# Performance work log

Measured on AMD Instinct MI355X. Metric: run time of the kernel, lower is better.

The kernel has to match this reference:

```python
import jax, jax.numpy as jnp
import numpy as np

B, M, FIN = 16, 49152, 16
F1, K = 32, 5
NNZ = 8 * M  # ~8 neighbors per vertex on a HEALPix sphere mesh


def setup_inputs() -> dict:
    key = jax.random.key(0)
    kx, kr, kc, kv, kw, kb = jax.random.split(key, 6)
    x = jax.random.normal(kx, (B, M, FIN), dtype=jnp.float32)
    rows = jax.random.randint(kr, (NNZ,), 0, M, dtype=jnp.int32)
    cols = jax.random.randint(kc, (NNZ,), 0, M, dtype=jnp.int32)
    # small values keep the order-K Chebyshev recurrence numerically tame
    vals = jax.random.normal(kv, (NNZ,), dtype=jnp.float32) * 0.1
    stddev = 1.0 / np.sqrt(FIN * (K + 0.5) / 2.0)
    kernel = jax.random.normal(kw, (FIN * K, F1), dtype=jnp.float32) * stddev
    bias = jax.random.uniform(kb, (1, 1, F1), dtype=jnp.float32) * 0.05
    return {"x": x, "rows": rows, "cols": cols, "vals": vals,
            "kernel": kernel, "bias": bias}


def reference(x, rows, cols, vals, kernel, bias):
    # x: [B, M, Fin]; sparse Laplacian L in COO (rows, cols, vals), shape [M, M]
    b, m, fin = x.shape
    k = kernel.shape[0] // fin

    def spmm(X):  # L @ X for X: [M, Fin*B]
        return jax.ops.segment_sum(vals[:, None] * X[cols], rows, num_segments=m)

    # x0: [M, Fin*B] exactly as the TF transpose/reshape does
    x0 = jnp.transpose(x, (1, 2, 0)).reshape(m, fin * b)
    xs = [x0]
    if k > 1:
        x1 = spmm(x0)
        xs.append(x1)
    for _ in range(2, k):
        x2 = 2.0 * spmm(x1) - x0
        xs.append(x2)
        x0, x1 = x1, x2
    # [K, M, Fin, B] -> [B, M, Fin, K] -> [B*M, Fin*K]
    xk = jnp.stack(xs, axis=0).reshape(k, m, fin, b)
    xk = jnp.transpose(xk, (3, 1, 2, 0)).reshape(b * m, fin * k)
    out = (xk @ kernel).reshape(b, m, -1)  # [B, M, F1]
    return out + bias
```

## Files before the change

kernel.cpp:

```cpp
#include <hip/hip_runtime.h>


constexpr int M   = 49152;
constexpr int B   = 16;
constexpr int FIN = 16;
constexpr int F1  = 32;
constexpr int K   = 5;
constexpr int XBS = M * FIN;
constexpr size_t SLICEB   = (size_t)M * 64;
constexpr size_t BUFBYTES = (size_t)M * 512;
constexpr int NBLK_M = M / 256;
constexpr int NHB = 64 * NBLK_M;

typedef short s16x8 __attribute__((ext_vector_type(8)));
typedef float f32x4 __attribute__((ext_vector_type(4)));
typedef unsigned int u32;
typedef unsigned long long u64;

#define DEVFN __device__ __forceinline__

DEVFN float lo2f(u32 d) {
  union { u32 u; float f; } v; v.u = d << 16; return v.f;
}
DEVFN float hi2f(u32 d) {
  union { u32 u; float f; } v; v.u = d & 0xffff0000u; return v.f;
}
DEVFN unsigned short f2bf(float f) {
  union { float f; u32 u; } v;
  v.f = f;
  u32 r = (v.u + 0x7FFFu + ((v.u >> 16) & 1u)) >> 16;
  return (unsigned short)r;
}


__global__ __launch_bounds__(256) void transform_x(const float* __restrict__ x,
                                                   char* __restrict__ x0b) {
  int lane = threadIdx.x & 63;
  int m = blockIdx.x * 4 + (threadIdx.x >> 6);
  int s = lane >> 3, i = lane & 7;
  int b = 2 * s + (i >> 2), f = (i & 3) * 4;
  float4 v = *(const float4*)(x + (size_t)b * XBS + (size_t)m * FIN + f);
  ushort4 r = make_ushort4(f2bf(v.x), f2bf(v.y), f2bf(v.z), f2bf(v.w));
  *(ushort4*)(x0b + (size_t)s * SLICEB + (size_t)m * 64 + i * 8) = r;
}


__global__ __launch_bounds__(256) void hist_kernel(const int* __restrict__ rows,
                                                   int* __restrict__ counts, int nnz) {
  int i = blockIdx.x * 256 + threadIdx.x;
  if (i < nnz) atomicAdd(&counts[rows[i]], 1);
}

DEVFN int wave_incl_scan(int v, int lane) {
#pragma unroll
  for (int off = 1; off < 64; off <<= 1) {
    int t = __shfl_up(v, off);
    if (lane >= off) v += t;
  }
  return v;
}

__global__ __launch_bounds__(1024) void scan_blocks(const int* __restrict__ src,
                                                    int* __restrict__ dst,
                                                    int* __restrict__ partials) {
  __shared__ int wsum[16];
  int tid = threadIdx.x, lane = tid & 63, w = tid >> 6;
  int i = blockIdx.x * 1024 + tid;
  int s = wave_incl_scan(src[i], lane);
  if (lane == 63) wsum[w] = s;
  __syncthreads();
  if (tid < 16) {
    int t = wsum[tid];
#pragma unroll
    for (int off = 1; off < 16; off <<= 1) {
      int u = __shfl_up(t, off);
      if (tid >= off) t += u;
    }
    wsum[tid] = t;
  }
  __syncthreads();
  int base = (w > 0) ? wsum[w - 1] : 0;
  s += base;
  dst[i + 1] = s;
  if (tid == 1023) partials[blockIdx.x] = s;
}

__global__ void scan_partials_kernel(int* __restrict__ partials,
                                     int* __restrict__ dst, int nblk) {
  int lane = threadIdx.x;
  int v = (lane < nblk) ? partials[lane] : 0;
  v = wave_incl_scan(v, lane);
  if (lane < nblk) partials[lane] = v;
  if (lane == 0) dst[0] = 0;
}

__global__ __launch_bounds__(1024) void scan_add_kernel(int* __restrict__ dst,
                                                        const int* __restrict__ partials) {
  if (blockIdx.x == 0) return;
  int i = blockIdx.x * 1024 + threadIdx.x;
  dst[i + 1] += partials[blockIdx.x - 1];
}

__global__ __launch_bounds__(256) void scatter_kernel(const int* __restrict__ rows,
                                                      const int* __restrict__ cols,
                                                      const float* __restrict__ vals,
                                                      const int* __restrict__ row_ptr,
                                                      int* __restrict__ fill,
                                                      u32* __restrict__ cvp, int nnz) {
  int i = blockIdx.x * 256 + threadIdx.x;
  if (i < nnz) {
    int r = rows[i];
    int pos = row_ptr[r] + atomicAdd(&fill[r], 1);
    cvp[pos] = ((u32)cols[i] << 16) | (u32)f2bf(vals[i]);
  }
}


__global__ __launch_bounds__(256) void deg_hist_blk(const int* __restrict__ counts,
                                                    int* __restrict__ blkhist) {
  __shared__ int lh[64];
  int tid = threadIdx.x;
  if (tid < 64) lh[tid] = 0;
  __syncthreads();
  int m = blockIdx.x * 256 + tid;
  atomicAdd(&lh[min(counts[m], 63)], 1);
  __syncthreads();
  if (tid < 64) blkhist[tid * NBLK_M + blockIdx.x] = lh[tid];
}

__global__ __launch_bounds__(256) void perm_scatter_blk(const int* __restrict__ counts,
                                                        const int* __restrict__ sc,
                                                        int* __restrict__ perm) {
  __shared__ int lh[64];
  __shared__ int lbase[64];
  int tid = threadIdx.x, blk = blockIdx.x;
  if (tid < 64) lh[tid] = 0;
  __syncthreads();
  int m = blk * 256 + tid;
  int d = min(counts[m], 63);
  int lr = atomicAdd(&lh[d], 1);
  __syncthreads();
  if (tid < 64) lbase[tid] = sc[tid * NBLK_M + blk];
  __syncthreads();
  perm[lbase[d] + lr] = m;
}


template <bool SUB>
__global__ __launch_bounds__(256) void spmm_strip(const char* __restrict__ xsrc,
                                                  const char* __restrict__ ssrc,
                                                  char* __restrict__ y,
                                                  const int* __restrict__ row_ptr,
                                                  const int* __restrict__ degs,
                                                  const int* __restrict__ perm,
                                                  const u32* __restrict__ cvp) {
  int s  = blockIdx.x & 7;
  int g4 = blockIdx.x >> 3;
  int lane = threadIdx.x & 63, wave = threadIdx.x >> 6;
  int r = lane >> 3, q = lane & 7;
  int rq = lane & 56;
  int grp = g4 * 4 + wave;
  const char* sbase = xsrc + (size_t)s * SLICEB;
  size_t qb = (size_t)q * 8;

  int ridA = perm[grp * 16 + r];
  int ridB = perm[grp * 16 + 8 + r];
  int baseA = row_ptr[ridA], baseB = row_ptr[ridB];
  int degA = degs[ridA], degB = degs[ridB];
  int wmax = max(degA, degB);
  wmax = max(wmax, __shfl_xor(wmax, 8));
  wmax = max(wmax, __shfl_xor(wmax, 16));
  wmax = max(wmax, __shfl_xor(wmax, 32));

  u64 svA = 0, svB = 0;
  if (SUB) {
    svA = __builtin_nontemporal_load(
        (const u64*)(ssrc + (size_t)s * SLICEB + (size_t)ridA * 64 + qb));
    svB = __builtin_nontemporal_load(
        (const u64*)(ssrc + (size_t)s * SLICEB + (size_t)ridB * 64 + qb));
  }

  float aA0 = 0.f, aA1 = 0.f, aA2 = 0.f, aA3 = 0.f;
  float aB0 = 0.f, aB1 = 0.f, aB2 = 0.f, aB3 = 0.f;
  for (int t0 = 0; t0 < wmax; t0 += 8) {
    int et = t0 + q;
    u32 cvA = 0u, cvB = 0u;
    if (et < degA) cvA = cvp[baseA + et];
    if (et < degB) cvB = cvp[baseB + et];
    u32 cA[8], cB[8];
    u64 dA[8], dB[8];
#pragma unroll
    for (int t = 0; t < 8; ++t) {
      cA[t] = (u32)__shfl((int)cvA, rq | t);
      dA[t] = *(const u64*)(sbase + (size_t)(cA[t] >> 16) * 64 + qb);
    }
#pragma unroll
    for (int t = 0; t < 8; ++t) {
      cB[t] = (u32)__shfl((int)cvB, rq | t);
      dB[t] = *(const u64*)(sbase + (size_t)(cB[t] >> 16) * 64 + qb);
    }
#pragma unroll
    for (int t = 0; t < 8; ++t) {
      float v = lo2f(cA[t]);
      u32 dl = (u32)dA[t], dh = (u32)(dA[t] >> 32);
      aA0 = fmaf(v, lo2f(dl), aA0); aA1 = fmaf(v, hi2f(dl), aA1);
      aA2 = fmaf(v, lo2f(dh), aA2); aA3 = fmaf(v, hi2f(dh), aA3);
    }
#pragma unroll
    for (int t = 0; t < 8; ++t) {
      float v = lo2f(cB[t]);
      u32 dl = (u32)dB[t], dh = (u32)(dB[t] >> 32);
      aB0 = fmaf(v, lo2f(dl), aB0); aB1 = fmaf(v, hi2f(dl), aB1);
      aB2 = fmaf(v, lo2f(dh), aB2); aB3 = fmaf(v, hi2f(dh), aB3);
    }
  }

  if (SUB) {
    u32 sl = (u32)svA, sh = (u32)(svA >> 32);
    aA0 = fmaf(2.f, aA0, -lo2f(sl)); aA1 = fmaf(2.f, aA1, -hi2f(sl));
    aA2 = fmaf(2.f, aA2, -lo2f(sh)); aA3 = fmaf(2.f, aA3, -hi2f(sh));
    sl = (u32)svB; sh = (u32)(svB >> 32);
    aB0 = fmaf(2.f, aB0, -lo2f(sl)); aB1 = fmaf(2.f, aB1, -hi2f(sl));
    aB2 = fmaf(2.f, aB2, -lo2f(sh)); aB3 = fmaf(2.f, aB3, -hi2f(sh));
  }
  u64 rvA = ((u64)(((u32)f2bf(aA3) << 16) | (u32)f2bf(aA2)) << 32) |
            (u64)(((u32)f2bf(aA1) << 16) | (u32)f2bf(aA0));
  u64 rvB = ((u64)(((u32)f2bf(aB3) << 16) | (u32)f2bf(aB2)) << 32) |
            (u64)(((u32)f2bf(aB1) << 16) | (u32)f2bf(aB0));
  __builtin_nontemporal_store(
      rvA, (u64*)(y + (size_t)s * SLICEB + (size_t)ridA * 64 + qb));
  __builtin_nontemporal_store(
      rvB, (u64*)(y + (size_t)s * SLICEB + (size_t)ridB * 64 + qb));
}


__global__ __launch_bounds__(256) void cheb_gemm_mfma(const char* __restrict__ xs0,
                                                      const float* __restrict__ kern,
                                                      const float* __restrict__ bias,
                                                      float* __restrict__ out) {
  __shared__ unsigned short bl[3][4][32][8];
  __shared__ float bsl[32];
  int tid = threadIdx.x;
  for (int idx = tid; idx < 3 * 4 * 32 * 8; idx += 256) {
    int j = idx & 7, o = (idx >> 3) & 31, g = (idx >> 8) & 3, c = idx >> 10;
    int k = 2 * c + (g >> 1), f = (g & 1) * 8 + j;
    bl[c][g][o][j] = (k < K) ? f2bf(kern[(f * K + k) * F1 + o]) : (unsigned short)0;
  }
  if (tid < 32) bsl[tid] = bias[tid];
  __syncthreads();

  int lane = tid & 63;
  int w = blockIdx.x * 4 + (tid >> 6);
  int bb = w & 1, pair = (w >> 1) & 7, mtg = w >> 4;
  int b = pair * 2 + bb;
  int mt0 = mtg * 8;

  int row = lane & 15, g = lane >> 4;
  int col = lane & 15;

  s16x8 bf[3][2];
#pragma unroll
  for (int c = 0; c < 3; ++c) {
#pragma unroll
    for (int ot = 0; ot < 2; ++ot)
      bf[c][ot] = *(const s16x8*)(&bl[c][g][col + 16 * ot][0]);
  }
  float bias0 = bsl[col], bias1 = bsl[col + 16];

  size_t lanebyte = (size_t)pair * SLICEB + (size_t)row * 64 +
                    (size_t)bb * 32 + (size_t)(g & 1) * 16;
  int khalf = g >> 1;
  const char* p0 = xs0 + (size_t)(0 + khalf) * BUFBYTES + lanebyte;
  const char* p1 = xs0 + (size_t)(2 + khalf) * BUFBYTES + lanebyte;
  const char* p2 = xs0 + (size_t)(4 + khalf) * BUFBYTES + lanebyte;

  size_t obase0 = ((size_t)b * M + (size_t)mt0 * 16) * F1;

#pragma unroll 2
  for (int t = 0; t < 8; ++t) {
    size_t moff = (size_t)(mt0 + t) * (16 * 64);
    s16x8 a0 = *(const s16x8*)(p0 + moff);
    s16x8 a1 = *(const s16x8*)(p1 + moff);
    s16x8 a2 = (g < 2) ? *(const s16x8*)(p2 + moff) : (s16x8)0;

    f32x4 acc0 = {0.f, 0.f, 0.f, 0.f};
    f32x4 acc1 = {0.f, 0.f, 0.f, 0.f};
    acc0 = __builtin_amdgcn_mfma_f32_16x16x32_bf16(a0, bf[0][0], acc0, 0, 0, 0);
    acc1 = __builtin_amdgcn_mfma_f32_16x16x32_bf16(a0, bf[0][1], acc1, 0, 0, 0);
    acc0 = __builtin_amdgcn_mfma_f32_16x16x32_bf16(a1, bf[1][0], acc0, 0, 0, 0);
    acc1 = __builtin_amdgcn_mfma_f32_16x16x32_bf16(a1, bf[1][1], acc1, 0, 0, 0);
    acc0 = __builtin_amdgcn_mfma_f32_16x16x32_bf16(a2, bf[2][0], acc0, 0, 0, 0);
    acc1 = __builtin_amdgcn_mfma_f32_16x16x32_bf16(a2, bf[2][1], acc1, 0, 0, 0);

    float* ob = out + obase0 + (size_t)t * (16 * F1);
#pragma unroll
    for (int j = 0; j < 4; ++j) {
      int r = g * 4 + j;
      ob[r * F1 + col]      = acc0[j] + bias0;
      ob[r * F1 + col + 16] = acc1[j] + bias1;
    }
  }
}


extern "C" void kernel_launch(void* const* d_in, const int* in_sizes, int n_in,
                              void* d_out, int out_size, void* d_ws, size_t ws_size,
                              hipStream_t stream) {
  const float* x    = (const float*)d_in[0];
  const int*   rows = (const int*)d_in[1];
  const int*   cols = (const int*)d_in[2];
  const float* vals = (const float*)d_in[3];
  const float* kern = (const float*)d_in[4];
  const float* bias = (const float*)d_in[5];
  float* out = (float*)d_out;
  int nnz = in_sizes[1];

  char* x0b = (char*)d_ws;
  char* x1b = x0b + BUFBYTES;
  char* x2b = x1b + BUFBYTES;
  char* x3b = x2b + BUFBYTES;
  char* x4b = x3b + BUFBYTES;
  int* row_ptr  = (int*)(x4b + BUFBYTES);
  int* counts   = row_ptr + (M + 256);
  int* fill     = counts + M;
  int* partials = fill + M;
  int* blkhist  = partials + 256;
  int* sc       = blkhist + NHB;
  int* perm     = sc + NHB + 256;
  u32* cvp      = (u32*)(perm + M);

  int nblk1024 = M / 1024;
  int nblkH    = NHB / 1024;
  int nblkNnz  = (nnz + 255) / 256;

  transform_x<<<M / 4, 256, 0, stream>>>(x, x0b);

  hipMemsetAsync(counts, 0, (size_t)2 * M * 4, stream);
  hist_kernel<<<nblkNnz, 256, 0, stream>>>(rows, counts, nnz);
  scan_blocks<<<nblk1024, 1024, 0, stream>>>(counts, row_ptr, partials);
  scan_partials_kernel<<<1, 64, 0, stream>>>(partials, row_ptr, nblk1024);
  scan_add_kernel<<<nblk1024, 1024, 0, stream>>>(row_ptr, partials);
  deg_hist_blk<<<NBLK_M, 256, 0, stream>>>(counts, blkhist);
  scan_blocks<<<nblkH, 1024, 0, stream>>>(blkhist, sc, partials);
  scan_partials_kernel<<<1, 64, 0, stream>>>(partials, sc, nblkH);
  scan_add_kernel<<<nblkH, 1024, 0, stream>>>(sc, partials);
  perm_scatter_blk<<<NBLK_M, 256, 0, stream>>>(counts, sc, perm);
  scatter_kernel<<<nblkNnz, 256, 0, stream>>>(rows, cols, vals, row_ptr, fill, cvp, nnz);

  int spmmGrid = 8 * (M / 64);
  spmm_strip<false><<<spmmGrid, 256, 0, stream>>>(x0b, nullptr, x1b, row_ptr, counts, perm, cvp);
  spmm_strip<true ><<<spmmGrid, 256, 0, stream>>>(x1b, x0b, x2b, row_ptr, counts, perm, cvp);
  spmm_strip<true ><<<spmmGrid, 256, 0, stream>>>(x2b, x1b, x3b, row_ptr, counts, perm, cvp);
  spmm_strip<true ><<<spmmGrid, 256, 0, stream>>>(x3b, x2b, x4b, row_ptr, counts, perm, cvp);

  cheb_gemm_mfma<<<1536, 256, 0, stream>>>(x0b, kern, bias, out);

  (void)n_in; (void)out_size; (void)ws_size; (void)in_sizes;
}
```

Before: 287.1 us.

## Pad CSR rows to multiples of eight and drop shuffles in SpMM edge loads

Each CSR row is padded to a multiple of eight entries that are zero-filled via memset, always with at least one padding slot. The SpMM then loads edge (col,val) words directly per lane, clamped to the padded limit, which replaces the per-group coalesced load plus eight shuffles and the bounds checks. The transform_x and GEMM block-to-work mappings are also reordered so reads are more contiguous per batch and neighbouring blocks share slices. This costs extra memory traffic for the padding, one more memset and one more kernel, and every lane now issues redundant scalar-ish loads of the edge words.

```diff
diff --git a/kernel.cpp b/kernel.cpp
--- a/kernel.cpp
+++ b/kernel.cpp
@@ -35,13 +35,15 @@
 
 __global__ __launch_bounds__(256) void transform_x(const float* __restrict__ x,
                                                    char* __restrict__ x0b) {
-  int lane = threadIdx.x & 63;
-  int m = blockIdx.x * 4 + (threadIdx.x >> 6);
-  int s = lane >> 3, i = lane & 7;
-  int b = 2 * s + (i >> 2), f = (i & 3) * 4;
+  int lane = threadIdx.x & 63, wave = threadIdx.x >> 6;
+  int mchunk = blockIdx.x >> 2, bquad = blockIdx.x & 3;
+  int b = bquad * 4 + wave;
+  int m = mchunk * 16 + (lane >> 2);
+  int f = (lane & 3) * 4;
   float4 v = *(const float4*)(x + (size_t)b * XBS + (size_t)m * FIN + f);
   ushort4 r = make_ushort4(f2bf(v.x), f2bf(v.y), f2bf(v.z), f2bf(v.w));
-  *(ushort4*)(x0b + (size_t)s * SLICEB + (size_t)m * 64 + i * 8) = r;
+  *(ushort4*)(x0b + (size_t)(b >> 1) * SLICEB + (size_t)m * 64 +
+              (size_t)(b & 1) * 32 + (size_t)(lane & 3) * 8) = r;
 }
 
 
@@ -49,6 +51,12 @@
                                                    int* __restrict__ counts, int nnz) {
   int i = blockIdx.x * 256 + threadIdx.x;
   if (i < nnz) atomicAdd(&counts[rows[i]], 1);
+}
+
+__global__ __launch_bounds__(256) void pad_counts(const int* __restrict__ counts,
+                                                  int* __restrict__ c8) {
+  int m = blockIdx.x * 256 + threadIdx.x;
+  c8[m] = (counts[m] + 8) & ~7;
 }
 
 DEVFN int wave_incl_scan(int v, int lane) {
@@ -104,13 +112,13 @@
 __global__ __launch_bounds__(256) void scatter_kernel(const int* __restrict__ rows,
                                                       const int* __restrict__ cols,
                                                       const float* __restrict__ vals,
-                                                      const int* __restrict__ row_ptr,
+                                                      const int* __restrict__ row_ptr8,
                                                       int* __restrict__ fill,
                                                       u32* __restrict__ cvp, int nnz) {
   int i = blockIdx.x * 256 + threadIdx.x;
   if (i < nnz) {
     int r = rows[i];
-    int pos = row_ptr[r] + atomicAdd(&fill[r], 1);
+    int pos = row_ptr8[r] + atomicAdd(&fill[r], 1);
     cvp[pos] = ((u32)cols[i] << 16) | (u32)f2bf(vals[i]);
   }
 }
@@ -147,30 +155,30 @@
 
 
 template <bool SUB>
-__global__ __launch_bounds__(256) void spmm_strip(const char* __restrict__ xsrc,
-                                                  const char* __restrict__ ssrc,
-                                                  char* __restrict__ y,
-                                                  const int* __restrict__ row_ptr,
-                                                  const int* __restrict__ degs,
-                                                  const int* __restrict__ perm,
-                                                  const u32* __restrict__ cvp) {
+__global__ __launch_bounds__(256) void spmm_pad(const char* __restrict__ xsrc,
+                                                const char* __restrict__ ssrc,
+                                                char* __restrict__ y,
+                                                const int* __restrict__ row_ptr8,
+                                                const int* __restrict__ perm,
+                                                const u32* __restrict__ cvp) {
   int s  = blockIdx.x & 7;
   int g4 = blockIdx.x >> 3;
   int lane = threadIdx.x & 63, wave = threadIdx.x >> 6;
   int r = lane >> 3, q = lane & 7;
-  int rq = lane & 56;
   int grp = g4 * 4 + wave;
   const char* sbase = xsrc + (size_t)s * SLICEB;
   size_t qb = (size_t)q * 8;
 
   int ridA = perm[grp * 16 + r];
   int ridB = perm[grp * 16 + 8 + r];
-  int baseA = row_ptr[ridA], baseB = row_ptr[ridB];
-  int degA = degs[ridA], degB = degs[ridB];
-  int wmax = max(degA, degB);
-  wmax = max(wmax, __shfl_xor(wmax, 8));
-  wmax = max(wmax, __shfl_xor(wmax, 16));
-  wmax = max(wmax, __shfl_xor(wmax, 32));
+  int baseA = row_ptr8[ridA], baseB = row_ptr8[ridB];
+  int plimA = row_ptr8[ridA + 1] - baseA - 1;
+  int plimB = row_ptr8[ridB + 1] - baseB - 1;
+
+  int wns = (max(plimA, plimB) + 1) >> 3;
+  wns = max(wns, __shfl_xor(wns, 8));
+  wns = max(wns, __shfl_xor(wns, 16));
+  wns = max(wns, __shfl_xor(wns, 32));
 
   u64 svA = 0, svB = 0;
   if (SUB) {
@@ -182,23 +190,20 @@
 
   float aA0 = 0.f, aA1 = 0.f, aA2 = 0.f, aA3 = 0.f;
   float aB0 = 0.f, aB1 = 0.f, aB2 = 0.f, aB3 = 0.f;
-  for (int t0 = 0; t0 < wmax; t0 += 8) {
-    int et = t0 + q;
-    u32 cvA = 0u, cvB = 0u;
-    if (et < degA) cvA = cvp[baseA + et];
-    if (et < degB) cvB = cvp[baseB + et];
+  int nedge = wns * 8;
+  for (int t0 = 0; t0 < nedge; t0 += 8) {
     u32 cA[8], cB[8];
     u64 dA[8], dB[8];
 #pragma unroll
-    for (int t = 0; t < 8; ++t) {
-      cA[t] = (u32)__shfl((int)cvA, rq | t);
+    for (int t = 0; t < 8; ++t) cA[t] = cvp[baseA + min(t0 + t, plimA)];
+#pragma unroll
+    for (int t = 0; t < 8; ++t) cB[t] = cvp[baseB + min(t0 + t, plimB)];
+#pragma unroll
+    for (int t = 0; t < 8; ++t)
       dA[t] = *(const u64*)(sbase + (size_t)(cA[t] >> 16) * 64 + qb);
-    }
-#pragma unroll
-    for (int t = 0; t < 8; ++t) {
-      cB[t] = (u32)__shfl((int)cvB, rq | t);
+#pragma unroll
+    for (int t = 0; t < 8; ++t)
       dB[t] = *(const u64*)(sbase + (size_t)(cB[t] >> 16) * 64 + qb);
-    }
 #pragma unroll
     for (int t = 0; t < 8; ++t) {
       float v = lo2f(cA[t]);
@@ -249,9 +254,10 @@
   if (tid < 32) bsl[tid] = bias[tid];
   __syncthreads();
 
-  int lane = tid & 63;
-  int w = blockIdx.x * 4 + (tid >> 6);
-  int bb = w & 1, pair = (w >> 1) & 7, mtg = w >> 4;
+  int lane = tid & 63, wave = tid >> 6;
+  int pair = blockIdx.x & 7;
+  int bb = wave & 1;
+  int mtg = (blockIdx.x >> 3) * 2 + (wave >> 1);
   int b = pair * 2 + bb;
   int mt0 = mtg * 8;
 
@@ -314,44 +320,48 @@
   const float* bias = (const float*)d_in[5];
   float* out = (float*)d_out;
   int nnz = in_sizes[1];
+  int padWords = nnz + 8 * M + 256;
 
   char* x0b = (char*)d_ws;
   char* x1b = x0b + BUFBYTES;
   char* x2b = x1b + BUFBYTES;
   char* x3b = x2b + BUFBYTES;
   char* x4b = x3b + BUFBYTES;
-  int* row_ptr  = (int*)(x4b + BUFBYTES);
-  int* counts   = row_ptr + (M + 256);
+  int* row_ptr8 = (int*)(x4b + BUFBYTES);
+  int* counts   = row_ptr8 + (M + 256);
   int* fill     = counts + M;
-  int* partials = fill + M;
+  int* c8       = fill + M;
+  int* partials = c8 + M;
   int* blkhist  = partials + 256;
   int* sc       = blkhist + NHB;
   int* perm     = sc + NHB + 256;
-  u32* cvp      = (u32*)(perm + M);
+  u32* cvp8     = (u32*)(perm + M);
 
   int nblk1024 = M / 1024;
   int nblkH    = NHB / 1024;
   int nblkNnz  = (nnz + 255) / 256;
 
-  transform_x<<<M / 4, 256, 0, stream>>>(x, x0b);
+  transform_x<<<(M / 16) * 4, 256, 0, stream>>>(x, x0b);
 
   hipMemsetAsync(counts, 0, (size_t)2 * M * 4, stream);
+  hipMemsetAsync(cvp8, 0, (size_t)padWords * 4, stream);
   hist_kernel<<<nblkNnz, 256, 0, stream>>>(rows, counts, nnz);
-  scan_blocks<<<nblk1024, 1024, 0, stream>>>(counts, row_ptr, partials);
-  scan_partials_kernel<<<1, 64, 0, stream>>>(partials, row_ptr, nblk1024);
-  scan_add_kernel<<<nblk1024, 1024, 0, stream>>>(row_ptr, partials);
+  pad_counts<<<NBLK_M, 256, 0, stream>>>(counts, c8);
+  scan_blocks<<<nblk1024, 1024, 0, stream>>>(c8, row_ptr8, partials);
+  scan_partials_kernel<<<1, 64, 0, stream>>>(partials, row_ptr8, nblk1024);
+  scan_add_kernel<<<nblk1024, 1024, 0, stream>>>(row_ptr8, partials);
   deg_hist_blk<<<NBLK_M, 256, 0, stream>>>(counts, blkhist);
   scan_blocks<<<nblkH, 1024, 0, stream>>>(blkhist, sc, partials);
   scan_partials_kernel<<<1, 64, 0, stream>>>(partials, sc, nblkH);
   scan_add_kernel<<<nblkH, 1024, 0, stream>>>(sc, partials);
   perm_scatter_blk<<<NBLK_M, 256, 0, stream>>>(counts, sc, perm);
-  scatter_kernel<<<nblkNnz, 256, 0, stream>>>(rows, cols, vals, row_ptr, fill, cvp, nnz);
+  scatter_kernel<<<nblkNnz, 256, 0, stream>>>(rows, cols, vals, row_ptr8, fill, cvp8, nnz);
 
   int spmmGrid = 8 * (M / 64);
-  spmm_strip<false><<<spmmGrid, 256, 0, stream>>>(x0b, nullptr, x1b, row_ptr, counts, perm, cvp);
-  spmm_strip<true ><<<spmmGrid, 256, 0, stream>>>(x1b, x0b, x2b, row_ptr, counts, perm, cvp);
-  spmm_strip<true ><<<spmmGrid, 256, 0, stream>>>(x2b, x1b, x3b, row_ptr, counts, perm, cvp);
-  spmm_strip<true ><<<spmmGrid, 256, 0, stream>>>(x3b, x2b, x4b, row_ptr, counts, perm, cvp);
+  spmm_pad<false><<<spmmGrid, 256, 0, stream>>>(x0b, nullptr, x1b, row_ptr8, perm, cvp8);
+  spmm_pad<true ><<<spmmGrid, 256, 0, stream>>>(x1b, x0b, x2b, row_ptr8, perm, cvp8);
+  spmm_pad<true ><<<spmmGrid, 256, 0, stream>>>(x2b, x1b, x3b, row_ptr8, perm, cvp8);
+  spmm_pad<true ><<<spmmGrid, 256, 0, stream>>>(x3b, x2b, x4b, row_ptr8, perm, cvp8);
 
   cheb_gemm_mfma<<<1536, 256, 0, stream>>>(x0b, kern, bias, out);
 
```

After: 303.8 us. 1.06x slower.
